# Kernel tuning notes

Hardware: AMD Instinct MI355X
Metric: run time of the kernel (lower is better)

Reference implementation:

```python
import jax, jax.numpy as jnp
import numpy as np

B, N, DIM, H, DH, PD = 2, 1024, 768, 8, 64, 4
EPS = 1e-8


def setup_inputs() -> dict:
    key = jax.random.key(0)
    ks = jax.random.split(key, 12)
    w = lambda k, shp: jax.random.normal(k, shp, dtype=jnp.float32) * 0.02
    return {
        "x": jax.random.normal(ks[0], (B, N, DIM), dtype=jnp.float32),
        "rotations": jax.random.normal(ks[1], (B, N, 3, 3), dtype=jnp.float32),
        "translations": jax.random.normal(ks[2], (B, N, 3), dtype=jnp.float32),
        "W_sq": w(ks[3], (H * DH, DIM)),
        "W_sk": w(ks[4], (H * DH, DIM)),
        "W_sv": w(ks[5], (H * DH, DIM)),
        "W_pq": w(ks[6], (H * PD * 3, DIM)),
        "W_pk": w(ks[7], (H * PD * 3, DIM)),
        "W_pv": w(ks[8], (H * PD * 3, DIM)),
        "point_weights": jax.random.normal(ks[9], (H,), dtype=jnp.float32),
        "W_out": w(ks[10], (DIM, H * (DH + PD * 4))),
        "b_out": jax.random.normal(ks[11], (DIM,), dtype=jnp.float32) * 0.02,
    }


def reference(x, rotations, translations, W_sq, W_sk, W_sv, W_pq, W_pk, W_pv, point_weights, W_out, b_out):
    b, n, _ = x.shape
    h, dh, pd = H, DH, PD
    scalar_scale = (2 * dh) ** -0.5           # num_attn_logits=2
    point_scale = (2 * pd * (9 / 2)) ** -0.5

    # scalar q/k/v: [b,h,n,dh]
    qs = (x @ W_sq.T).reshape(b, n, h, dh).transpose(0, 2, 1, 3)
    ks = (x @ W_sk.T).reshape(b, n, h, dh).transpose(0, 2, 1, 3)
    vs = (x @ W_sv.T).reshape(b, n, h, dh).transpose(0, 2, 1, 3)

    # point q/k/v: [b,h,n,pd,3]
    qp = (x @ W_pq.T).reshape(b, n, h, pd, 3).transpose(0, 2, 1, 3, 4)
    kp = (x @ W_pk.T).reshape(b, n, h, pd, 3).transpose(0, 2, 1, 3, 4)
    vp = (x @ W_pv.T).reshape(b, n, h, pd, 3).transpose(0, 2, 1, 3, 4)

    t = translations[:, None, :, None, :]  # [b,1,n,1,3]
    # global-frame points: p_c = sum_r R[n,c,r] * p[d,r] + t
    qp = jnp.einsum('bncr,bhndr->bhndc', rotations, qp) + t
    kp = jnp.einsum('bncr,bhndr->bhndc', rotations, kp) + t
    vp = jnp.einsum('bncr,bhndr->bhndc', rotations, vp) + t

    # scalar attention logits [b,h,i,j]
    logits = jnp.einsum('bhid,bhjd->bhij', qs, ks) * scalar_scale

    # point distance term: sum_{d,c} (q-k)^2 = |q|^2 + |k|^2 - 2 q.k (no [i,j,d,c] tensor)
    q2 = jnp.sum(qp ** 2, axis=(-1, -2))  # [b,h,i]
    k2 = jnp.sum(kp ** 2, axis=(-1, -2))  # [b,h,j]
    qk = jnp.einsum('bhidc,bhjdc->bhij', qp, kp)
    point_dist = q2[..., :, None] + k2[..., None, :] - 2.0 * qk

    pw = jax.nn.softplus(point_weights)[None, :, None, None]  # [1,h,1,1]
    logits = logits - 0.5 * (point_dist * pw * point_scale)

    attn = jax.nn.softmax(logits, axis=-1)

    rs = jnp.einsum('bhij,bhjd->bhid', attn, vs)          # [b,h,n,dh]
    rp = jnp.einsum('bhij,bhjdc->bhidc', attn, vp)        # [b,h,n,pd,3]
    # back to local frame: R^T (p - t)
    rp = jnp.einsum('bnrc,bhndr->bhndc', rotations, rp - t)
    rn = jnp.sqrt(jnp.sum(rp ** 2, axis=-1) + EPS)        # [b,h,n,pd]

    rs = rs.transpose(0, 2, 1, 3).reshape(b, n, h * dh)
    rp_f = rp.transpose(0, 2, 1, 3, 4).reshape(b, n, h * pd * 3)
    rn = rn.transpose(0, 2, 1, 3).reshape(b, n, h * pd)

    results = jnp.concatenate([rs, rp_f, rn], axis=-1)    # [b,n,640]
    return results @ W_out.T + b_out
```

## Files before the change

kernel.cpp:

```cpp
#include <hip/hip_runtime.h>
#include <hip/hip_bf16.h>
#include <math.h>

#define B_  2
#define N_  1024
#define DIM_ 768
#define H_  8
#define DH_ 64
#define PD_ 4
#define NPROJ 1824
#define NPAD  1920
#define BH_ (B_*H_)
#define FDIM 640

#define OFF_RS   0u
#define OFF_RP   (OFF_RS + (size_t)BH_*N_*DH_)
#define OFF_PRAW (OFF_RP + (size_t)BH_*N_*12)
#define OFF_QA   (OFF_PRAW + (size_t)B_*N_*288)
#define OFF_KA   (OFF_QA + (size_t)BH_*N_*96/2)
#define OFF_VT   (OFF_KA + (size_t)BH_*N_*96/2)
#define OFF_XB   (OFF_VT + (size_t)BH_*80*N_/2)
#define OFF_WB   (OFF_XB + (size_t)B_*N_*DIM_/2)
#define OFF_FB   OFF_XB
#define OFF_WOB  OFF_WB

typedef __attribute__((ext_vector_type(8))) short bf16x8;
typedef __attribute__((ext_vector_type(4))) float f32x4;

__device__ __forceinline__ unsigned short f2bf(float f) {
    __hip_bfloat16 h = __float2bfloat16(f);
    return *reinterpret_cast<unsigned short*>(&h);
}

__device__ __forceinline__ unsigned long long pack4(
    unsigned short a, unsigned short b, unsigned short c, unsigned short d)
{
    return (unsigned long long)a
         | ((unsigned long long)b << 16)
         | ((unsigned long long)c << 32)
         | ((unsigned long long)d << 48);
}

#define GLOAD(dst, ptr) \
    asm volatile("global_load_dwordx4 %0, %1, off" \
                 : "=v"(dst) : "v"(ptr) : "memory")

__global__ __launch_bounds__(256) void k_cvt_x(
    const float* __restrict__ x, unsigned short* __restrict__ xb)
{
    int i = blockIdx.x * 256 + threadIdx.x;
    if (i >= (B_*N_*DIM_)/4) return;
    float4 v = reinterpret_cast<const float4*>(x)[i];
    reinterpret_cast<unsigned long long*>(xb)[i] =
        pack4(f2bf(v.x), f2bf(v.y), f2bf(v.z), f2bf(v.w));
}

__global__ __launch_bounds__(256) void k_cvt_w(
    const float* __restrict__ Wsq, const float* __restrict__ Wsk,
    const float* __restrict__ Wsv, const float* __restrict__ Wpq,
    const float* __restrict__ Wpk, const float* __restrict__ Wpv,
    unsigned short* __restrict__ wb)
{
    int i = blockIdx.x * 256 + threadIdx.x;
    if (i >= (NPAD*DIM_)/4) return;
    int row = i / (DIM_/4);
    int c4  = i % (DIM_/4);
    unsigned long long o;
    if (row >= NPROJ) {
        o = 0ull;
    } else {
        const float* W;
        if      (row < 512)  W = Wsq + (size_t)row*DIM_;
        else if (row < 1024) W = Wsk + (size_t)(row-512)*DIM_;
        else if (row < 1536) W = Wsv + (size_t)(row-1024)*DIM_;
        else if (row < 1632) W = Wpq + (size_t)(row-1536)*DIM_;
        else if (row < 1728) W = Wpk + (size_t)(row-1632)*DIM_;
        else                 W = Wpv + (size_t)(row-1728)*DIM_;
        float4 v = reinterpret_cast<const float4*>(W)[c4];
        o = pack4(f2bf(v.x), f2bf(v.y), f2bf(v.z), f2bf(v.w));
    }
    reinterpret_cast<unsigned long long*>(wb)[i] = o;
}

__global__ __launch_bounds__(256) void k_cvt_wout(
    const float* __restrict__ Wout, unsigned short* __restrict__ wob)
{
    int i = blockIdx.x * 256 + threadIdx.x;
    if (i >= (DIM_*FDIM)/4) return;
    float4 v = reinterpret_cast<const float4*>(Wout)[i];
    reinterpret_cast<unsigned long long*>(wob)[i] =
        pack4(f2bf(v.x), f2bf(v.y), f2bf(v.z), f2bf(v.w));
}

__global__ __launch_bounds__(64, 4) void k_proj_mfma(
    const unsigned short* __restrict__ xb,
    const unsigned short* __restrict__ wb,
    float* __restrict__ ws)
{
    const int lane = threadIdx.x;
    const int lo = lane & 15;
    const int hi = lane >> 4;
    const int bid = blockIdx.x;
    const int L = (bid & 7)*480 + (bid >> 3);
    const int mt = L / 60;
    const int nt = L % 60;
    const int row0 = mt*32;
    const int col0 = nt*32;

    const char* pA0 = (const char*)(xb + (size_t)(row0 + lo)*DIM_ + hi*8);
    const char* pA1 = pA0 + (size_t)16*DIM_*2;
    const char* pB0 = (const char*)(wb + (size_t)(col0 + lo)*DIM_ + hi*8);
    const char* pB1 = pB0 + (size_t)16*DIM_*2;

    f32x4 acc[2][2];
    #pragma unroll
    for (int m = 0; m < 2; ++m)
        #pragma unroll
        for (int n = 0; n < 2; ++n) acc[m][n] = (f32x4){0.f,0.f,0.f,0.f};

    bf16x8 bA0[4], bA1[4], bB0[4], bB1[4];
    #pragma unroll
    for (int s = 0; s < 4; ++s) {
        GLOAD(bA0[s], pA0 + s*64);
        GLOAD(bA1[s], pA1 + s*64);
        GLOAD(bB0[s], pB0 + s*64);
        GLOAD(bB1[s], pB1 + s*64);
    }
    #pragma unroll
    for (int kt = 0; kt < 20; ++kt) {
        const int s = kt & 3;
        asm volatile("s_waitcnt vmcnt(12)" ::: "memory");
        __builtin_amdgcn_sched_barrier(0);
        acc[0][0] = __builtin_amdgcn_mfma_f32_16x16x32_bf16(bA0[s], bB0[s], acc[0][0], 0, 0, 0);
        acc[0][1] = __builtin_amdgcn_mfma_f32_16x16x32_bf16(bA0[s], bB1[s], acc[0][1], 0, 0, 0);
        acc[1][0] = __builtin_amdgcn_mfma_f32_16x16x32_bf16(bA1[s], bB0[s], acc[1][0], 0, 0, 0);
        acc[1][1] = __builtin_amdgcn_mfma_f32_16x16x32_bf16(bA1[s], bB1[s], acc[1][1], 0, 0, 0);
        __builtin_amdgcn_sched_barrier(0);
        const int kn = kt + 4;
        GLOAD(bA0[s], pA0 + kn*64);
        GLOAD(bA1[s], pA1 + kn*64);
        GLOAD(bB0[s], pB0 + kn*64);
        GLOAD(bB1[s], pB1 + kn*64);
    }
    #define PROJ_TAIL(kt, W) { \
        const int s = (kt) & 3; \
        asm volatile("s_waitcnt vmcnt(" #W ")" ::: "memory"); \
        __builtin_amdgcn_sched_barrier(0); \
        acc[0][0] = __builtin_amdgcn_mfma_f32_16x16x32_bf16(bA0[s], bB0[s], acc[0][0], 0, 0, 0); \
        acc[0][1] = __builtin_amdgcn_mfma_f32_16x16x32_bf16(bA0[s], bB1[s], acc[0][1], 0, 0, 0); \
        acc[1][0] = __builtin_amdgcn_mfma_f32_16x16x32_bf16(bA1[s], bB0[s], acc[1][0], 0, 0, 0); \
        acc[1][1] = __builtin_amdgcn_mfma_f32_16x16x32_bf16(bA1[s], bB1[s], acc[1][1], 0, 0, 0); \
    }
    PROJ_TAIL(20, 12)
    PROJ_TAIL(21, 8)
    PROJ_TAIL(22, 4)
    PROJ_TAIL(23, 0)
    #undef PROJ_TAIL

    unsigned short* qa = (unsigned short*)(ws + OFF_QA);
    unsigned short* ka = (unsigned short*)(ws + OFF_KA);
    unsigned short* vt = (unsigned short*)(ws + OFF_VT);
    float* praw = ws + OFF_PRAW;
    const float ss = 0.08838834764831845f;

    #pragma unroll
    for (int n = 0; n < 2; ++n) {
        int o = col0 + n*16 + lo;
        if (o >= NPROJ) continue;
        if (o >= 1024 && o < 1536) {
            int oo = o - 1024; int h = oo >> 6, c = oo & 63;
            #pragma unroll
            for (int m = 0; m < 2; ++m) {
                int r0 = row0 + m*16 + hi*4;
                int bb = r0 >> 10, nn0 = r0 & (N_-1);
                unsigned long long pk = pack4(
                    f2bf(acc[m][n][0]), f2bf(acc[m][n][1]),
                    f2bf(acc[m][n][2]), f2bf(acc[m][n][3]));
                *reinterpret_cast<unsigned long long*>(
                    vt + ((size_t)(bb*H_ + h)*80 + c)*N_ + nn0) = pk;
            }
        } else {
            #pragma unroll
            for (int m = 0; m < 2; ++m) {
                #pragma unroll
                for (int j = 0; j < 4; ++j) {
                    int r = row0 + m*16 + hi*4 + j;
                    int bb = r >> 10, nn = r & (N_-1);
                    float v = acc[m][n][j];
                    if (o < 512) {
                        int h = o >> 6, c = o & 63;
                        qa[((size_t)(bb*H_ + h)*N_ + nn)*96 + c] = f2bf(v*ss);
                    } else if (o < 1024) {
                        int oo = o - 512; int h = oo >> 6, c = oo & 63;
                        ka[((size_t)(bb*H_ + h)*N_ + nn)*96 + c] = f2bf(v);
                    } else {
                        praw[(size_t)r*288 + (o - 1536)] = v;
                    }
                }
            }
        }
    }
}

__global__ __launch_bounds__(128) void k_prep(
    const float* __restrict__ rot_g,
    const float* __restrict__ trans_g,
    const float* __restrict__ pw_g,
    float* __restrict__ ws)
{
    __shared__ float R[9], T[3];
    __shared__ float rot[3][8][4][3];
    __shared__ float p2[2][8][4];
    __shared__ float q2t[8], k2t[8], coefs[8];
    const int tid = threadIdx.x;
    const int row = blockIdx.x;
    const int b = row >> 10, n = row & (N_-1);

    if (tid < 9)  R[tid] = rot_g[(size_t)row*9 + tid];
    if (tid >= 9 && tid < 12) T[tid-9] = trans_g[(size_t)row*3 + (tid-9)];
    if (tid >= 16 && tid < 24) {
        float pw = pw_g[tid-16];
        coefs[tid-16] = 0.5f * log1pf(__expf(pw)) * (1.0f/6.0f);
    }
    __syncthreads();
    if (tid < 96) {
        int which = tid >> 5, idx = tid & 31;
        int h = idx >> 2, pd = idx & 3;
        const float* p = ws + OFF_PRAW + (size_t)row*288 + which*96 + h*12 + pd*3;
        float px = p[0], py = p[1], pz = p[2];
        float c0 = R[0]*px + R[1]*py + R[2]*pz + T[0];
        float c1 = R[3]*px + R[4]*py + R[5]*pz + T[1];
        float c2 = R[6]*px + R[7]*py + R[8]*pz + T[2];
        rot[which][h][pd][0] = c0;
        rot[which][h][pd][1] = c1;
        rot[which][h][pd][2] = c2;
        if (which < 2) p2[which][h][pd] = c0*c0 + c1*c1 + c2*c2;
    }
    __syncthreads();
    if (tid < 16) {
        int w = tid >> 3, h = tid & 7;
        float s = p2[w][h][0] + p2[w][h][1] + p2[w][h][2] + p2[w][h][3];
        if (w) k2t[h] = s; else q2t[h] = s;
    }
    __syncthreads();

    unsigned short* qa = (unsigned short*)(ws + OFF_QA);
    unsigned short* ka = (unsigned short*)(ws + OFF_KA);
    unsigned short* vt = (unsigned short*)(ws + OFF_VT);

    for (int i = tid; i < 256; i += 128) {
        int h = i >> 5, c = i & 31;
        float qv, kv;
        if (c < 12)      { qv = rot[0][h][c/3][c%3] * 2.f * coefs[h]; kv = rot[1][h][c/3][c%3]; }
        else if (c == 12){ qv = q2t[h];  kv = -coefs[h]; }
        else if (c == 13){ qv = 1.f;     kv = -coefs[h]*k2t[h]; }
        else             { qv = 0.f;     kv = 0.f; }
        size_t base = ((size_t)(b*H_ + h)*N_ + n)*96 + 64 + c;
        qa[base] = f2bf(qv);
        ka[base] = f2bf(kv);
    }
    {
        int h = tid >> 4, r = tid & 15;
        float vv = (r < 12) ? rot[2][h][r/3][r%3] : 0.f;
        vt[((size_t)(b*H_ + h)*80 + 64 + r)*N_ + n] = f2bf(vv);
    }
}

#define VPAD 72
#define APAD 84
__global__ __launch_bounds__(512, 4) void k_attn_mfma(
    const unsigned short* __restrict__ qa_g,
    const unsigned short* __restrict__ ka_g,
    const unsigned short* __restrict__ vt_g,
    float* __restrict__ ws)
{
    __shared__ unsigned short sP[8][16*VPAD];
    __shared__ float sAcc[3][2][16][APAD];
    __shared__ float sML[3][2][16][2];

    const int tid  = threadIdx.x;
    const int lane = tid & 63;
    const int wid  = tid >> 6;
    const int lo = lane & 15;
    const int hi = lane >> 4;
    const int bid = blockIdx.x;
    const int Lb = (bid & 7)*64 + (bid >> 3);
    const int bh = Lb >> 5;
    const int qt = Lb & 31;
    const int q0 = qt * 32;
    const int qh = wid & 1;
    const int kq = wid >> 1;
    const int mrow = qh * 16;

    const unsigned short* Qa = qa_g + (size_t)bh*N_*96;
    const unsigned short* Ka = ka_g + (size_t)bh*N_*96;
    const unsigned short* Vt = vt_g + (size_t)bh*80*N_;

    bf16x8 qfr[3];
    {
        int qrow = q0 + mrow + lo;
        #pragma unroll
        for (int c = 0; c < 3; ++c)
            qfr[c] = *reinterpret_cast<const bf16x8*>(
                Qa + (size_t)qrow*96 + c*32 + hi*8);
    }

    f32x4 acc[5];
    #pragma unroll
    for (int d = 0; d < 5; ++d) acc[d] = (f32x4){0.f,0.f,0.f,0.f};
    float m[4] = {-1e30f,-1e30f,-1e30f,-1e30f};
    float l[4] = {0.f,0.f,0.f,0.f};

    for (int it = 0; it < 4; ++it) {
        const int j0 = (kq*4 + it)*64;

        bf16x8 kb[3][4];
        #pragma unroll
        for (int c = 0; c < 3; ++c)
            #pragma unroll
            for (int t = 0; t < 4; ++t)
                kb[c][t] = *reinterpret_cast<const bf16x8*>(
                    Ka + (size_t)(j0 + t*16 + lo)*96 + c*32 + hi*8);

        f32x4 s[4];
        #pragma unroll
        for (int t = 0; t < 4; ++t) s[t] = (f32x4){0.f,0.f,0.f,0.f};
        #pragma unroll
        for (int c = 0; c < 3; ++c)
            #pragma unroll
            for (int t = 0; t < 4; ++t)
                s[t] = __builtin_amdgcn_mfma_f32_16x16x32_bf16(qfr[c], kb[c][t], s[t], 0, 0, 0);

        bf16x8 vb[2][5];
        #pragma unroll
        for (int kk = 0; kk < 2; ++kk)
            #pragma unroll
            for (int dt = 0; dt < 5; ++dt)
                vb[kk][dt] = *reinterpret_cast<const bf16x8*>(
                    Vt + (size_t)(dt*16 + lo)*N_ + j0 + kk*32 + hi*8);

        float scl[4];
        #pragma unroll
        for (int r = 0; r < 4; ++r) {
            float v = fmaxf(fmaxf(s[0][r], s[1][r]), fmaxf(s[2][r], s[3][r]));
            v = fmaxf(v, __shfl_xor(v, 1));
            v = fmaxf(v, __shfl_xor(v, 2));
            v = fmaxf(v, __shfl_xor(v, 4));
            v = fmaxf(v, __shfl_xor(v, 8));
            float mn = fmaxf(m[r], v);
            scl[r] = __expf(m[r] - mn);
            m[r] = mn;
        }
        float ps[4] = {0.f,0.f,0.f,0.f};
        #pragma unroll
        for (int t = 0; t < 4; ++t) {
            #pragma unroll
            for (int r = 0; r < 4; ++r) {
                float p = __expf(s[t][r] - m[r]);
                ps[r] += p;
                sP[wid][(hi*4 + r)*VPAD + t*16 + lo] = f2bf(p);
            }
        }
        #pragma unroll
        for (int r = 0; r < 4; ++r) {
            float v = ps[r];
            v += __shfl_xor(v, 1);
            v += __shfl_xor(v, 2);
            v += __shfl_xor(v, 4);
            v += __shfl_xor(v, 8);
            l[r] = l[r]*scl[r] + v;
        }
        #pragma unroll
        for (int d = 0; d < 5; ++d)
            #pragma unroll
            for (int r = 0; r < 4; ++r) acc[d][r] *= scl[r];

        #pragma unroll
        for (int kk = 0; kk < 2; ++kk) {
            bf16x8 pa = *reinterpret_cast<const bf16x8*>(
                &sP[wid][lo*VPAD + kk*32 + hi*8]);
            #pragma unroll
            for (int dt = 0; dt < 5; ++dt)
                acc[dt] = __builtin_amdgcn_mfma_f32_16x16x32_bf16(pa, vb[kk][dt], acc[dt], 0, 0, 0);
        }
    }

    if (kq > 0) {
        #pragma unroll
        for (int r = 0; r < 4; ++r) {
            int rl = hi*4 + r;
            #pragma unroll
            for (int dt = 0; dt < 5; ++dt)
                sAcc[kq-1][qh][rl][dt*16 + lo] = acc[dt][r];
            if (lo == 0) { sML[kq-1][qh][rl][0] = m[r]; sML[kq-1][qh][rl][1] = l[r]; }
        }
    }
    __syncthreads();
    if (kq == 0) {
        float* ws_rs = ws + OFF_RS + (size_t)bh*N_*DH_;
        float* ws_rp = ws + OFF_RP + (size_t)bh*N_*12;
        #pragma unroll
        for (int r = 0; r < 4; ++r) {
            int rl = hi*4 + r;
            float mp[3], lp[3];
            float mm = m[r];
            #pragma unroll
            for (int p = 0; p < 3; ++p) {
                mp[p] = sML[p][qh][rl][0];
                lp[p] = sML[p][qh][rl][1];
                mm = fmaxf(mm, mp[p]);
            }
            float f0 = __expf(m[r] - mm);
            float Lsum = l[r]*f0;
            float fp[3];
            #pragma unroll
            for (int p = 0; p < 3; ++p) {
                fp[p] = __expf(mp[p] - mm);
                Lsum += lp[p]*fp[p];
            }
            float inv = 1.f / Lsum;
            int i = q0 + mrow + rl;
            #pragma unroll
            for (int dt = 0; dt < 5; ++dt) {
                float val = acc[dt][r]*f0;
                #pragma unroll
                for (int p = 0; p < 3; ++p)
                    val += sAcc[p][qh][rl][dt*16 + lo]*fp[p];
                val *= inv;
                int d = dt*16 + lo;
                if (d < 64)
                    ws_rs[(size_t)i*DH_ + d] = val;
                else if (d - 64 < 12)
                    ws_rp[(size_t)i*12 + (d - 64)] = val;
            }
        }
    }
}

__global__ __launch_bounds__(256) void k_fin_prep(
    const float* __restrict__ rotations,
    const float* __restrict__ translations,
    const float* __restrict__ ws,
    unsigned short* __restrict__ fb)
{
    __shared__ float sF[8][FDIM];
    const int tid = threadIdx.x;
    const int row0 = blockIdx.x * 8;
    const int b = row0 >> 10;
    const float* ws_rs = ws + OFF_RS;
    const float* ws_rp = ws + OFF_RP;

    for (int i = tid; i < 8*512; i += 256) {
        int r = i >> 9, f = i & 511;
        int h = f >> 6, c = f & 63;
        int n = (row0 & (N_-1)) + r;
        sF[r][f] = ws_rs[(((size_t)(b*H_ + h))*N_ + n)*DH_ + c];
    }
    {
        int r = tid >> 5;
        int idx = tid & 31;
        int h = idx >> 2, pd = idx & 3;
        int row = row0 + r;
        int n = row & (N_-1);
        const float* rp = ws_rp + (((size_t)(b*H_ + h))*N_ + n)*12 + pd*3;
        const float* R = rotations + (size_t)row*9;
        const float* T = translations + (size_t)row*3;
        float d0 = rp[0] - T[0], d1 = rp[1] - T[1], d2 = rp[2] - T[2];
        float l0 = R[0]*d0 + R[3]*d1 + R[6]*d2;
        float l1 = R[1]*d0 + R[4]*d1 + R[7]*d2;
        float l2 = R[2]*d0 + R[5]*d1 + R[8]*d2;
        sF[r][512 + h*12 + pd*3 + 0] = l0;
        sF[r][512 + h*12 + pd*3 + 1] = l1;
        sF[r][512 + h*12 + pd*3 + 2] = l2;
        sF[r][608 + h*4 + pd] = sqrtf(l0*l0 + l1*l1 + l2*l2 + 1e-8f);
    }
    __syncthreads();

    #pragma unroll
    for (int r = 0; r < 8; ++r) {
        for (int f4 = tid; f4 < FDIM/4; f4 += 256) {
            unsigned long long pk = pack4(
                f2bf(sF[r][f4*4+0]), f2bf(sF[r][f4*4+1]),
                f2bf(sF[r][f4*4+2]), f2bf(sF[r][f4*4+3]));
            reinterpret_cast<unsigned long long*>(fb + (size_t)(row0 + r)*FDIM)[f4] = pk;
        }
    }
}

__global__ __launch_bounds__(64, 4) void k_out_mfma(
    const unsigned short* __restrict__ fb,
    const unsigned short* __restrict__ wob,
    const float* __restrict__ bout,
    float* __restrict__ out)
{
    const int lane = threadIdx.x;
    const int lo = lane & 15;
    const int hi = lane >> 4;
    const int bid = blockIdx.x;
    const int L = (bid & 7)*192 + (bid >> 3);
    const int mt = L / 24;
    const int nt = L % 24;
    const int row0 = mt*32;
    const int col0 = nt*32;

    const char* pA0 = (const char*)(fb  + (size_t)(row0 + lo)*FDIM + hi*8);
    const char* pA1 = pA0 + (size_t)16*FDIM*2;
    const char* pB0 = (const char*)(wob + (size_t)(col0 + lo)*FDIM + hi*8);
    const char* pB1 = pB0 + (size_t)16*FDIM*2;

    f32x4 acc[2][2];
    #pragma unroll
    for (int m = 0; m < 2; ++m)
        #pragma unroll
        for (int n = 0; n < 2; ++n) acc[m][n] = (f32x4){0.f,0.f,0.f,0.f};

    bf16x8 bA0[4], bA1[4], bB0[4], bB1[4];
    #pragma unroll
    for (int s = 0; s < 4; ++s) {
        GLOAD(bA0[s], pA0 + s*64);
        GLOAD(bA1[s], pA1 + s*64);
        GLOAD(bB0[s], pB0 + s*64);
        GLOAD(bB1[s], pB1 + s*64);
    }
    #pragma unroll
    for (int kt = 0; kt < 16; ++kt) {
        const int s = kt & 3;
        asm volatile("s_waitcnt vmcnt(12)" ::: "memory");
        __builtin_amdgcn_sched_barrier(0);
        acc[0][0] = __builtin_amdgcn_mfma_f32_16x16x32_bf16(bA0[s], bB0[s], acc[0][0], 0, 0, 0);
        acc[0][1] = __builtin_amdgcn_mfma_f32_16x16x32_bf16(bA0[s], bB1[s], acc[0][1], 0, 0, 0);
        acc[1][0] = __builtin_amdgcn_mfma_f32_16x16x32_bf16(bA1[s], bB0[s], acc[1][0], 0, 0, 0);
        acc[1][1] = __builtin_amdgcn_mfma_f32_16x16x32_bf16(bA1[s], bB1[s], acc[1][1], 0, 0, 0);
        __builtin_amdgcn_sched_barrier(0);
        const int kn = kt + 4;
        GLOAD(bA0[s], pA0 + kn*64);
        GLOAD(bA1[s], pA1 + kn*64);
        GLOAD(bB0[s], pB0 + kn*64);
        GLOAD(bB1[s], pB1 + kn*64);
    }
    #define OUT_TAIL(kt, W) { \
        const int s = (kt) & 3; \
        asm volatile("s_waitcnt vmcnt(" #W ")" ::: "memory"); \
        __builtin_amdgcn_sched_barrier(0); \
        acc[0][0] = __builtin_amdgcn_mfma_f32_16x16x32_bf16(bA0[s], bB0[s], acc[0][0], 0, 0, 0); \
        acc[0][1] = __builtin_amdgcn_mfma_f32_16x16x32_bf16(bA0[s], bB1[s], acc[0][1], 0, 0, 0); \
        acc[1][0] = __builtin_amdgcn_mfma_f32_16x16x32_bf16(bA1[s], bB0[s], acc[1][0], 0, 0, 0); \
        acc[1][1] = __builtin_amdgcn_mfma_f32_16x16x32_bf16(bA1[s], bB1[s], acc[1][1], 0, 0, 0); \
    }
    OUT_TAIL(16, 12)
    OUT_TAIL(17, 8)
    OUT_TAIL(18, 4)
    OUT_TAIL(19, 0)
    #undef OUT_TAIL

    #pragma unroll
    for (int n = 0; n < 2; ++n) {
        int o = col0 + n*16 + lo;
        float bo = bout[o];
        #pragma unroll
        for (int m = 0; m < 2; ++m) {
            #pragma unroll
            for (int j = 0; j < 4; ++j) {
                int r = row0 + m*16 + hi*4 + j;
                out[(size_t)r*DIM_ + o] = acc[m][n][j] + bo;
            }
        }
    }
}

extern "C" void kernel_launch(void* const* d_in, const int* in_sizes, int n_in,
                              void* d_out, int out_size, void* d_ws, size_t ws_size,
                              hipStream_t stream) {
    const float* x            = (const float*)d_in[0];
    const float* rotations    = (const float*)d_in[1];
    const float* translations = (const float*)d_in[2];
    const float* Wsq          = (const float*)d_in[3];
    const float* Wsk          = (const float*)d_in[4];
    const float* Wsv          = (const float*)d_in[5];
    const float* Wpq          = (const float*)d_in[6];
    const float* Wpk          = (const float*)d_in[7];
    const float* Wpv          = (const float*)d_in[8];
    const float* pweights     = (const float*)d_in[9];
    const float* Wout         = (const float*)d_in[10];
    const float* bout         = (const float*)d_in[11];
    float* out = (float*)d_out;
    float* ws  = (float*)d_ws;

    unsigned short* xb  = (unsigned short*)(ws + OFF_XB);
    unsigned short* wb  = (unsigned short*)(ws + OFF_WB);
    unsigned short* qa  = (unsigned short*)(ws + OFF_QA);
    unsigned short* ka  = (unsigned short*)(ws + OFF_KA);
    unsigned short* vt  = (unsigned short*)(ws + OFF_VT);
    unsigned short* fb  = (unsigned short*)(ws + OFF_FB);
    unsigned short* wob = (unsigned short*)(ws + OFF_WOB);

    k_cvt_x<<<(B_*N_*DIM_/4 + 255)/256, 256, 0, stream>>>(x, xb);
    k_cvt_w<<<(NPAD*DIM_/4 + 255)/256, 256, 0, stream>>>(Wsq, Wsk, Wsv, Wpq, Wpk, Wpv, wb);
    k_proj_mfma<<<3840, 64, 0, stream>>>(xb, wb, ws);
    k_prep<<<B_*N_, 128, 0, stream>>>(rotations, translations, pweights, ws);
    k_attn_mfma<<<BH_*32, 512, 0, stream>>>(qa, ka, vt, ws);
    k_cvt_wout<<<(DIM_*FDIM/4 + 255)/256, 256, 0, stream>>>(Wout, wob);
    k_fin_prep<<<B_*N_/8, 256, 0, stream>>>(rotations, translations, ws, fb);
    k_out_mfma<<<1536, 64, 0, stream>>>(fb, wob, bout, out);
}
```

Before: 118.7 us.

## Retile output GEMM with LDS staging, drop projection padding, swizzle x conversion

The output projection GEMM moves from 1536 single-wave 32x32 blocks that stream operands straight from global memory to 96 four-wave blocks. Each block computes a 128x128 tile and stages A/B k-slices in LDS through global_load_lds, so operands are reused across waves. The projection path also drops the zero-padded weight rows (NPAD 1920 down to NPROJ 1824), shrinking the grid to 3648 blocks, and the x-conversion kernel gets an XCD-style block swizzle. The new GEMM has only 96 blocks and no double buffering, so it may underfill the GPU and expose load latency.

```diff
diff --git a/kernel.cpp b/kernel.cpp
--- a/kernel.cpp
+++ b/kernel.cpp
@@ -9,7 +9,6 @@
 #define DH_ 64
 #define PD_ 4
 #define NPROJ 1824
-#define NPAD  1920
 #define BH_ (B_*H_)
 #define FDIM 640
 
@@ -48,7 +47,8 @@
 __global__ __launch_bounds__(256) void k_cvt_x(
     const float* __restrict__ x, unsigned short* __restrict__ xb)
 {
-    int i = blockIdx.x * 256 + threadIdx.x;
+    int bid = blockIdx.x;
+    int i = (((bid & 7) * 192) + (bid >> 3)) * 256 + threadIdx.x;
     if (i >= (B_*N_*DIM_)/4) return;
     float4 v = reinterpret_cast<const float4*>(x)[i];
     reinterpret_cast<unsigned long long*>(xb)[i] =
@@ -62,24 +62,19 @@
     unsigned short* __restrict__ wb)
 {
     int i = blockIdx.x * 256 + threadIdx.x;
-    if (i >= (NPAD*DIM_)/4) return;
+    if (i >= (NPROJ*DIM_)/4) return;
     int row = i / (DIM_/4);
     int c4  = i % (DIM_/4);
-    unsigned long long o;
-    if (row >= NPROJ) {
-        o = 0ull;
-    } else {
-        const float* W;
-        if      (row < 512)  W = Wsq + (size_t)row*DIM_;
-        else if (row < 1024) W = Wsk + (size_t)(row-512)*DIM_;
-        else if (row < 1536) W = Wsv + (size_t)(row-1024)*DIM_;
-        else if (row < 1632) W = Wpq + (size_t)(row-1536)*DIM_;
-        else if (row < 1728) W = Wpk + (size_t)(row-1632)*DIM_;
-        else                 W = Wpv + (size_t)(row-1728)*DIM_;
-        float4 v = reinterpret_cast<const float4*>(W)[c4];
-        o = pack4(f2bf(v.x), f2bf(v.y), f2bf(v.z), f2bf(v.w));
-    }
-    reinterpret_cast<unsigned long long*>(wb)[i] = o;
+    const float* W;
+    if      (row < 512)  W = Wsq + (size_t)row*DIM_;
+    else if (row < 1024) W = Wsk + (size_t)(row-512)*DIM_;
+    else if (row < 1536) W = Wsv + (size_t)(row-1024)*DIM_;
+    else if (row < 1632) W = Wpq + (size_t)(row-1536)*DIM_;
+    else if (row < 1728) W = Wpk + (size_t)(row-1632)*DIM_;
+    else                 W = Wpv + (size_t)(row-1728)*DIM_;
+    float4 v = reinterpret_cast<const float4*>(W)[c4];
+    reinterpret_cast<unsigned long long*>(wb)[i] =
+        pack4(f2bf(v.x), f2bf(v.y), f2bf(v.z), f2bf(v.w));
 }
 
 __global__ __launch_bounds__(256) void k_cvt_wout(
@@ -101,9 +96,9 @@
     const int lo = lane & 15;
     const int hi = lane >> 4;
     const int bid = blockIdx.x;
-    const int L = (bid & 7)*480 + (bid >> 3);
-    const int mt = L / 60;
-    const int nt = L % 60;
+    const int L = (bid & 7)*456 + (bid >> 3);
+    const int mt = L / 57;
+    const int nt = L % 57;
     const int row0 = mt*32;
     const int col0 = nt*32;
 
@@ -166,7 +161,6 @@
     #pragma unroll
     for (int n = 0; n < 2; ++n) {
         int o = col0 + n*16 + lo;
-        if (o >= NPROJ) continue;
         if (o >= 1024 && o < 1536) {
             int oo = o - 1024; int h = oo >> 6, c = oo & 63;
             #pragma unroll
@@ -487,81 +481,72 @@
     }
 }
 
-__global__ __launch_bounds__(64, 4) void k_out_mfma(
+__global__ __launch_bounds__(256) void k_out_mfma(
     const unsigned short* __restrict__ fb,
     const unsigned short* __restrict__ wob,
     const float* __restrict__ bout,
     float* __restrict__ out)
 {
-    const int lane = threadIdx.x;
-    const int lo = lane & 15;
-    const int hi = lane >> 4;
-    const int bid = blockIdx.x;
-    const int L = (bid & 7)*192 + (bid >> 3);
-    const int mt = L / 24;
-    const int nt = L % 24;
-    const int row0 = mt*32;
-    const int col0 = nt*32;
-
-    const char* pA0 = (const char*)(fb  + (size_t)(row0 + lo)*FDIM + hi*8);
-    const char* pA1 = pA0 + (size_t)16*FDIM*2;
-    const char* pB0 = (const char*)(wob + (size_t)(col0 + lo)*FDIM + hi*8);
-    const char* pB1 = pB0 + (size_t)16*FDIM*2;
-
-    f32x4 acc[2][2];
-    #pragma unroll
-    for (int m = 0; m < 2; ++m)
-        #pragma unroll
-        for (int n = 0; n < 2; ++n) acc[m][n] = (f32x4){0.f,0.f,0.f,0.f};
-
-    bf16x8 bA0[4], bA1[4], bB0[4], bB1[4];
-    #pragma unroll
-    for (int s = 0; s < 4; ++s) {
-        GLOAD(bA0[s], pA0 + s*64);
-        GLOAD(bA1[s], pA1 + s*64);
-        GLOAD(bB0[s], pB0 + s*64);
-        GLOAD(bB1[s], pB1 + s*64);
-    }
-    #pragma unroll
-    for (int kt = 0; kt < 16; ++kt) {
-        const int s = kt & 3;
-        asm volatile("s_waitcnt vmcnt(12)" ::: "memory");
-        __builtin_amdgcn_sched_barrier(0);
-        acc[0][0] = __builtin_amdgcn_mfma_f32_16x16x32_bf16(bA0[s], bB0[s], acc[0][0], 0, 0, 0);
-        acc[0][1] = __builtin_amdgcn_mfma_f32_16x16x32_bf16(bA0[s], bB1[s], acc[0][1], 0, 0, 0);
-        acc[1][0] = __builtin_amdgcn_mfma_f32_16x16x32_bf16(bA1[s], bB0[s], acc[1][0], 0, 0, 0);
-        acc[1][1] = __builtin_amdgcn_mfma_f32_16x16x32_bf16(bA1[s], bB1[s], acc[1][1], 0, 0, 0);
-        __builtin_amdgcn_sched_barrier(0);
-        const int kn = kt + 4;
-        GLOAD(bA0[s], pA0 + kn*64);
-        GLOAD(bA1[s], pA1 + kn*64);
-        GLOAD(bB0[s], pB0 + kn*64);
-        GLOAD(bB1[s], pB1 + kn*64);
-    }
-    #define OUT_TAIL(kt, W) { \
-        const int s = (kt) & 3; \
-        asm volatile("s_waitcnt vmcnt(" #W ")" ::: "memory"); \
-        __builtin_amdgcn_sched_barrier(0); \
-        acc[0][0] = __builtin_amdgcn_mfma_f32_16x16x32_bf16(bA0[s], bB0[s], acc[0][0], 0, 0, 0); \
-        acc[0][1] = __builtin_amdgcn_mfma_f32_16x16x32_bf16(bA0[s], bB1[s], acc[0][1], 0, 0, 0); \
-        acc[1][0] = __builtin_amdgcn_mfma_f32_16x16x32_bf16(bA1[s], bB0[s], acc[1][0], 0, 0, 0); \
-        acc[1][1] = __builtin_amdgcn_mfma_f32_16x16x32_bf16(bA1[s], bB1[s], acc[1][1], 0, 0, 0); \
-    }
-    OUT_TAIL(16, 12)
-    OUT_TAIL(17, 8)
-    OUT_TAIL(18, 4)
-    OUT_TAIL(19, 0)
-    #undef OUT_TAIL
-
-    #pragma unroll
-    for (int n = 0; n < 2; ++n) {
-        int o = col0 + n*16 + lo;
+    __shared__ unsigned short sAB[2*128*32];
+    const int tid  = threadIdx.x;
+    const int lane = tid & 63;
+    const int wid  = tid >> 6;
+    const int mt = blockIdx.x & 15;
+    const int nt = blockIdx.x >> 4;
+    const int row0 = mt*128;
+    const int col0 = nt*128;
+    const int wr = (wid >> 1)*64;
+    const int wc = (wid & 1)*64;
+
+    f32x4 acc[4][4];
+    #pragma unroll
+    for (int m = 0; m < 4; ++m)
+        #pragma unroll
+        for (int n = 0; n < 4; ++n) acc[m][n] = (f32x4){0.f,0.f,0.f,0.f};
+
+    for (int kt = 0; kt < FDIM/32; ++kt) {
+        __syncthreads();
+        #pragma unroll
+        for (int t = 0; t < 4; ++t) {
+            int chunk = t*4 + wid;
+            int tile  = chunk >> 3;
+            int crow  = (chunk & 7) * 16;
+            int grow  = (tile ? col0 : row0) + crow + (lane >> 2);
+            const unsigned short* gsrc = (tile ? wob : fb)
+                + (size_t)grow*FDIM + kt*32 + (lane & 3)*8;
+            __builtin_amdgcn_global_load_lds(
+                (const __attribute__((address_space(1))) void*)gsrc,
+                (__attribute__((address_space(3))) void*)(sAB + chunk*512),
+                16, 0, 0);
+        }
+        __syncthreads();
+
+        bf16x8 a[4], b[4];
+        #pragma unroll
+        for (int m = 0; m < 4; ++m)
+            a[m] = *reinterpret_cast<const bf16x8*>(
+                sAB + ((wr + m*16 + (lane & 15))*32 + (lane >> 4)*8));
+        #pragma unroll
+        for (int n = 0; n < 4; ++n)
+            b[n] = *reinterpret_cast<const bf16x8*>(
+                sAB + 128*32 + ((wc + n*16 + (lane & 15))*32 + (lane >> 4)*8));
+        #pragma unroll
+        for (int m = 0; m < 4; ++m)
+            #pragma unroll
+            for (int n = 0; n < 4; ++n)
+                acc[m][n] = __builtin_amdgcn_mfma_f32_16x16x32_bf16(
+                    a[m], b[n], acc[m][n], 0, 0, 0);
+    }
+
+    #pragma unroll
+    for (int n = 0; n < 4; ++n) {
+        int o = col0 + wc + n*16 + (lane & 15);
         float bo = bout[o];
         #pragma unroll
-        for (int m = 0; m < 2; ++m) {
+        for (int m = 0; m < 4; ++m) {
             #pragma unroll
             for (int j = 0; j < 4; ++j) {
-                int r = row0 + m*16 + hi*4 + j;
+                int r = row0 + wr + m*16 + (lane >> 4)*4 + j;
                 out[(size_t)r*DIM_ + o] = acc[m][n][j] + bo;
             }
         }
@@ -594,12 +579,12 @@
     unsigned short* fb  = (unsigned short*)(ws + OFF_FB);
     unsigned short* wob = (unsigned short*)(ws + OFF_WOB);
 
-    k_cvt_x<<<(B_*N_*DIM_/4 + 255)/256, 256, 0, stream>>>(x, xb);
-    k_cvt_w<<<(NPAD*DIM_/4 + 255)/256, 256, 0, stream>>>(Wsq, Wsk, Wsv, Wpq, Wpk, Wpv, wb);
-    k_proj_mfma<<<3840, 64, 0, stream>>>(xb, wb, ws);
+    k_cvt_x<<<1536, 256, 0, stream>>>(x, xb);
+    k_cvt_w<<<(NPROJ*DIM_/4 + 255)/256, 256, 0, stream>>>(Wsq, Wsk, Wsv, Wpq, Wpk, Wpv, wb);
+    k_proj_mfma<<<3648, 64, 0, stream>>>(xb, wb, ws);
     k_prep<<<B_*N_, 128, 0, stream>>>(rotations, translations, pweights, ws);
     k_attn_mfma<<<BH_*32, 512, 0, stream>>>(qa, ka, vt, ws);
     k_cvt_wout<<<(DIM_*FDIM/4 + 255)/256, 256, 0, stream>>>(Wout, wob);
     k_fin_prep<<<B_*N_/8, 256, 0, stream>>>(rotations, translations, ws, fb);
-    k_out_mfma<<<1536, 64, 0, stream>>>(fb, wob, bout, out);
-}
+    k_out_mfma<<<16*6, 256, 0, stream>>>(fb, wob, bout, out);
+}
```

Result: no change. 117.8 us (-0.7%).
